# Kernel optimization log

Hardware: AMD Instinct MI355X
Metric: run time of the kernel (lower is better)

The kernel has to match this reference:

```python
import jax, jax.numpy as jnp
import numpy as np
from jax import lax


def bilinear_resize(x, oh, ow):
    # x: (..., H, W); torch F.interpolate bilinear, align_corners=False
    H, W = x.shape[-2], x.shape[-1]
    def coords(n_in, n_out):
        src = (jnp.arange(n_out, dtype=jnp.float32) + 0.5) * (n_in / n_out) - 0.5
        src = jnp.clip(src, 0.0, n_in - 1.0)
        i0 = jnp.floor(src).astype(jnp.int32)
        i1 = jnp.minimum(i0 + 1, n_in - 1)
        return i0, i1, src - i0.astype(jnp.float32)
    r0, r1, wr = coords(H, oh)
    c0, c1, wc = coords(W, ow)
    xr = x[..., r0, :] * (1.0 - wr)[:, None] + x[..., r1, :] * wr[:, None]
    return xr[..., c0] * (1.0 - wc) + xr[..., c1] * wc


def setup_inputs():
    key = jax.random.key(0)
    ks = jax.random.split(key, 20)
    B, D, C, WIN, NH, A = 256, 1280, 64, 14, 8, 49
    def p(k, *sh):
        return jax.random.normal(k, sh, dtype=jnp.float32) * 0.02
    return {
        "X": jax.random.normal(ks[0], (B, 3, D), dtype=jnp.float32),
        "W_embed": p(ks[1], C * WIN * WIN, D), "b_embed": p(ks[2], C * WIN * WIN),
        "W_qkv": p(ks[3], 3 * C, C),
        "W_proj": p(ks[4], C, C), "b_proj": p(ks[5], C),
        "dwc_w": p(ks[6], C, 1, 3, 3), "dwc_b": p(ks[7], C),
        "an_bias": p(ks[8], NH, A, 7, 7), "na_bias": p(ks[9], NH, A, 7, 7),
        "ah_bias": p(ks[10], 1, NH, A, WIN, 1), "aw_bias": p(ks[11], 1, NH, A, 1, WIN),
        "ha_bias": p(ks[12], 1, NH, WIN, 1, A), "wa_bias": p(ks[13], 1, NH, 1, WIN, A),
        "W_adj": p(ks[14], 256, C * WIN * WIN), "b_adj": p(ks[15], 256),
        "W_t1": p(ks[16], 256, D), "b_t1": p(ks[17], 256),
        "W_t2": p(ks[18], 128, 256), "b_t2": p(ks[19], 128),
    }


def reference(X, W_embed, b_embed, W_qkv, W_proj, b_proj, dwc_w, dwc_b,
              an_bias, na_bias, ah_bias, aw_bias, ha_bias, wa_bias,
              W_adj, b_adj, W_t1, b_t1, W_t2, b_t2):
    B = X.shape[0]
    C, WIN, NH, A = 64, 14, 8, 49
    N = WIN * WIN            # 196 tokens
    HD = C // NH             # head dim 8
    scale = HD ** -0.5
    b3 = 3 * B

    # embed_to_img: (B*3, 1280) -> (B*3, C*N) -> tokens (B*3, N, C)
    Xe = X.reshape(b3, -1) @ W_embed.T + b_embed
    xt = Xe.reshape(b3, N, C)

    # AgentAttention
    qkv = xt @ W_qkv.T                                  # (b3, N, 3C), qkv_bias=False
    q, k, v = jnp.split(qkv, 3, axis=-1)
    # agent tokens: AdaptiveAvgPool2d 14x14 -> 7x7 over q (exact 2x2 mean)
    agent = q.reshape(b3, 7, 2, 7, 2, C).mean(axis=(2, 4)).reshape(b3, A, C)
    q = q.reshape(b3, N, NH, HD).transpose(0, 2, 1, 3)
    k = k.reshape(b3, N, NH, HD).transpose(0, 2, 1, 3)
    v = v.reshape(b3, N, NH, HD).transpose(0, 2, 1, 3)
    agent = agent.reshape(b3, A, NH, HD).transpose(0, 2, 1, 3)

    # stage 1: agents attend to all tokens
    pb = bilinear_resize(an_bias, WIN, WIN).reshape(NH, A, N) \
         + (ah_bias + aw_bias).reshape(NH, A, N)
    agent_attn = jax.nn.softmax(jnp.einsum('bhad,bhnd->bhan', agent * scale, k) + pb, axis=-1)
    agent_v = jnp.einsum('bhan,bhnd->bhad', agent_attn, v)   # (b3, NH, A, HD)

    # stage 2: tokens attend to agents
    ab = bilinear_resize(na_bias, WIN, WIN).reshape(NH, A, N).transpose(0, 2, 1) \
         + (ha_bias + wa_bias).reshape(NH, N, A)
    q_attn = jax.nn.softmax(jnp.einsum('bhnd,bhad->bhna', q * scale, agent) + ab, axis=-1)
    o = jnp.einsum('bhna,bhad->bhnd', q_attn, agent_v)
    o = o.transpose(0, 2, 1, 3).reshape(b3, N, C)

    # depthwise conv enhancement on v
    v_img = v.transpose(0, 2, 1, 3).reshape(b3, WIN, WIN, C).transpose(0, 3, 1, 2)
    dwc = lax.conv_general_dilated(v_img, dwc_w, (1, 1), [(1, 1), (1, 1)],
                                   feature_group_count=C) + dwc_b[None, :, None, None]
    o = o + dwc.transpose(0, 2, 3, 1).reshape(b3, N, C)
    o = o @ W_proj.T + b_proj

    X_adj = (o.reshape(b3, -1) @ W_adj.T + b_adj).reshape(B, 3, -1)

    def mlp(z):
        return jnp.tanh(z @ W_t1.T + b_t1) @ W_t2.T + b_t2
    anchor, pos, neg = mlp(X[:, 0]), mlp(X[:, 1]), mlp(X[:, 2])
    return anchor, pos, neg, X_adj
```

## Files before the change

kernel.cpp:

```cpp
#include <hip/hip_runtime.h>

using u16 = unsigned short;
using u32 = unsigned int;

constexpr int Bn   = 256;
constexpr int Dd   = 1280;
constexpr int Cc   = 64;
constexpr int WINc = 14;
constexpr int NHc  = 8;
constexpr int Ac   = 49;
constexpr int Nc   = WINc * WINc;
constexpr int HDc  = Cc / NHc;
constexpr int B3c  = 3 * Bn;
constexpr int CNc  = Cc * Nc;

typedef __attribute__((ext_vector_type(8))) short v8s;
typedef __attribute__((ext_vector_type(4))) float v4f;
typedef __attribute__((ext_vector_type(2))) float v2f;

__device__ __forceinline__ float bflo(u32 u){ union{u32 x; float f;} c; c.x = u << 16; return c.f; }
__device__ __forceinline__ float bfhi(u32 u){ union{u32 x; float f;} c; c.x = u & 0xffff0000u; return c.f; }
__device__ __forceinline__ float bfs(u16 h){ union{u32 x; float f;} c; c.x = ((u32)h) << 16; return c.f; }
__device__ __forceinline__ u16 f2bb(float f){
  u32 u = __float_as_uint(f);
  u32 r = (u + 0x7fffu + ((u >> 16) & 1u)) >> 16;
  return (u16)r;
}
__device__ __forceinline__ void unpack8(uint4 u, float* dst){
  dst[0]=bflo(u.x); dst[1]=bfhi(u.x); dst[2]=bflo(u.y); dst[3]=bfhi(u.y);
  dst[4]=bflo(u.z); dst[5]=bfhi(u.z); dst[6]=bflo(u.w); dst[7]=bfhi(u.w);
}
__device__ __forceinline__ uint4 pack8(const float* s){
  uint4 r;
  r.x = (u32)f2bb(s[0]) | ((u32)f2bb(s[1]) << 16);
  r.y = (u32)f2bb(s[2]) | ((u32)f2bb(s[3]) << 16);
  r.z = (u32)f2bb(s[4]) | ((u32)f2bb(s[5]) << 16);
  r.w = (u32)f2bb(s[6]) | ((u32)f2bb(s[7]) << 16);
  return r;
}

__device__ __forceinline__ void gl_lds16(const u16* g, u16* l){
  __builtin_amdgcn_global_load_lds(
      (const __attribute__((address_space(1))) unsigned int*)g,
      (__attribute__((address_space(3))) unsigned int*)l,
      16, 0, 0);
}

constexpr int WeN   = 12544 * 1280;
constexpr int XN    = 768 * 1280;
constexpr int WadjN = 256 * CNc;
constexpr int W1N   = 256 * 1280;
constexpr int W2N   = 128 * 256;
constexpr int CONVB = (WeN + XN + WadjN + W1N + W2N) / (256*8);
constexpr int BIASB = (2 * NHc * Ac * Nc + 255) / 256;
__global__ __launch_bounds__(256) void conv_bias_kernel(const float* __restrict__ We,
                                                        const float* __restrict__ X,
                                                        const float* __restrict__ Wadj,
                                                        const float* __restrict__ W1,
                                                        const float* __restrict__ W2,
                                                        u16* __restrict__ WeB,
                                                        u16* __restrict__ XB,
                                                        u16* __restrict__ WadjB,
                                                        u16* __restrict__ W1B,
                                                        u16* __restrict__ W2B,
                                                        const float* __restrict__ an, const float* __restrict__ na,
                                                        const float* __restrict__ ah, const float* __restrict__ aw,
                                                        const float* __restrict__ ha, const float* __restrict__ wa,
                                                        float* __restrict__ pb, float* __restrict__ ab)
{
  if (blockIdx.x >= CONVB) {
    const int total = NHc * Ac * Nc;
    int idx = (blockIdx.x - CONVB) * 256 + threadIdx.x;
    if (idx >= 2 * total) return;
    const bool isab = idx >= total;
    const int r = isab ? idx - total : idx;
    const int h = r / (Ac * Nc);
    const int r2 = r % (Ac * Nc);
    int a, n;
    if (isab) { n = r2 / Ac; a = r2 % Ac; } else { a = r2 / Nc; n = r2 % Nc; }
    const int y = n / WINc, x = n % WINc;
    float sy = fminf(fmaxf(0.5f * y - 0.25f, 0.f), 6.f);
    float sx = fminf(fmaxf(0.5f * x - 0.25f, 0.f), 6.f);
    const int y0 = (int)sy, x0 = (int)sx;
    const float wy = sy - y0, wx = sx - x0;
    const int y1 = (y0 + 1 < 6) ? y0 + 1 : 6;
    const int x1 = (x0 + 1 < 6) ? x0 + 1 : 6;
    const float* src = (isab ? na : an) + (h * Ac + a) * 49;
    const float v00 = src[y0*7 + x0], v01 = src[y0*7 + x1];
    const float v10 = src[y1*7 + x0], v11 = src[y1*7 + x1];
    const float bi = (1.f - wy) * ((1.f - wx) * v00 + wx * v01)
                   + wy * ((1.f - wx) * v10 + wx * v11);
    if (!isab) pb[((size_t)h*Nc + n)*Ac + a] = bi + ah[(h*Ac + a)*WINc + y] + aw[(h*Ac + a)*WINc + x];
    else       ab[((size_t)h*Ac + a)*Nc + n] = bi + ha[(h*WINc + y)*Ac + a] + wa[(h*WINc + x)*Ac + a];
    return;
  }
  const size_t idx = ((size_t)blockIdx.x * 256 + threadIdx.x) * 8;
  const float* src; u16* dst;
  if (idx < (size_t)WeN)                          { src = We + idx;                         dst = WeB + idx; }
  else if (idx < (size_t)WeN + XN)                { src = X + (idx - WeN);                  dst = XB + (idx - WeN); }
  else if (idx < (size_t)WeN + XN + WadjN)        { src = Wadj + (idx - WeN - XN);          dst = WadjB + (idx - WeN - XN); }
  else if (idx < (size_t)WeN + XN + WadjN + W1N)  { src = W1 + (idx - WeN - XN - WadjN);    dst = W1B + (idx - WeN - XN - WadjN); }
  else                                            { src = W2 + (idx - WeN - XN - WadjN - W1N); dst = W2B + (idx - WeN - XN - WadjN - W1N); }
  float v[8];
  *reinterpret_cast<float4*>(&v[0]) = *reinterpret_cast<const float4*>(src);
  *reinterpret_cast<float4*>(&v[4]) = *reinterpret_cast<const float4*>(src + 4);
  *reinterpret_cast<uint4*>(dst) = pack8(v);
}

template<int KK, int NN, bool TANH>
__global__ __launch_bounds__(256) void gemm_bf16_t(const u16* __restrict__ Amat,
                                                   const u16* __restrict__ Bmat,
                                                   const float* __restrict__ bias,
                                                   u16* __restrict__ Cmat)
{
  __shared__ u16 As[128 * 32];
  __shared__ u16 Bs[128 * 32];
  const int t = threadIdx.x;
  const int n0 = blockIdx.x * 128, m0 = blockIdx.y * 128;
  const int wave = t >> 6, lane = t & 63;
  const int wm = wave >> 1, wn = wave & 1;
  const int mi = lane & 15, quad = lane >> 4;

  v4f acc[4][4];
  #pragma unroll
  for (int a = 0; a < 4; ++a)
    #pragma unroll
    for (int b = 0; b < 4; ++b) acc[a][b] = (v4f){0.f, 0.f, 0.f, 0.f};

  const int rs = wave*32 + (lane >> 2);
  const int cs = (lane & 3) * 8;
  const u16* ga0 = Amat + (size_t)(m0 + rs) * KK + cs;
  const u16* ga1 = Amat + (size_t)(m0 + rs + 16) * KK + cs;
  const u16* gb0 = Bmat + (size_t)(n0 + rs) * KK + cs;
  const u16* gb1 = Bmat + (size_t)(n0 + rs + 16) * KK + cs;
  u16* la0 = &As[(wave*32)      * 32];
  u16* la1 = &As[(wave*32 + 16) * 32];
  u16* lb0 = &Bs[(wave*32)      * 32];
  u16* lb1 = &Bs[(wave*32 + 16) * 32];

  for (int kt = 0; kt < KK; kt += 32) {
    gl_lds16(ga0 + kt, la0);
    gl_lds16(ga1 + kt, la1);
    gl_lds16(gb0 + kt, lb0);
    gl_lds16(gb1 + kt, lb1);
    __syncthreads();

    v8s af[4], bf[4];
    #pragma unroll
    for (int mt = 0; mt < 4; ++mt)
      af[mt] = *reinterpret_cast<const v8s*>(&As[(wm*64 + mt*16 + mi)*32 + quad*8]);
    #pragma unroll
    for (int nt = 0; nt < 4; ++nt)
      bf[nt] = *reinterpret_cast<const v8s*>(&Bs[(wn*64 + nt*16 + mi)*32 + quad*8]);
    #pragma unroll
    for (int mt = 0; mt < 4; ++mt)
      #pragma unroll
      for (int nt = 0; nt < 4; ++nt)
        acc[mt][nt] = __builtin_amdgcn_mfma_f32_16x16x32_bf16(af[mt], bf[nt], acc[mt][nt], 0, 0, 0);
    __syncthreads();
  }

  #pragma unroll
  for (int nt = 0; nt < 4; ++nt) {
    const int col = n0 + wn*64 + nt*16 + mi;
    const float bc = bias[col];
    #pragma unroll
    for (int mt = 0; mt < 4; ++mt) {
      #pragma unroll
      for (int r = 0; r < 4; ++r) {
        const int row = m0 + wm*64 + mt*16 + quad*4 + r;
        float val = acc[mt][nt][r] + bc;
        if constexpr (TANH) val = tanhf(val);
        Cmat[(size_t)row * NN + col] = f2bb(val);
      }
    }
  }
}

__global__ __launch_bounds__(256) void mlp2_mfma(const u16* __restrict__ H,
                                                 const u16* __restrict__ W2B,
                                                 const float* __restrict__ b2,
                                                 float* __restrict__ outp)
{
  __shared__ u16 As[128 * 40];
  __shared__ u16 Bs[128 * 40];
  const int t = threadIdx.x;
  const int m0 = blockIdx.x * 128;
  const int wave = t >> 6, lane = t & 63;
  const int wm = wave >> 1, wn = wave & 1;
  const int mi = lane & 15, quad = lane >> 4;
  const int srow = t >> 1, scol = (t & 1) * 16;

  v4f acc[4][4];
  #pragma unroll
  for (int a = 0; a < 4; ++a)
    #pragma unroll
    for (int b = 0; b < 4; ++b) acc[a][b] = (v4f){0.f, 0.f, 0.f, 0.f};

  for (int kt = 0; kt < 256; kt += 32) {
    const u16* ap = H + (size_t)(m0 + srow) * 256 + kt + scol;
    *reinterpret_cast<uint4*>(&As[srow*40 + scol])     = *reinterpret_cast<const uint4*>(ap);
    *reinterpret_cast<uint4*>(&As[srow*40 + scol + 8]) = *reinterpret_cast<const uint4*>(ap + 8);
    const u16* bp = W2B + (size_t)srow * 256 + kt + scol;
    *reinterpret_cast<uint4*>(&Bs[srow*40 + scol])     = *reinterpret_cast<const uint4*>(bp);
    *reinterpret_cast<uint4*>(&Bs[srow*40 + scol + 8]) = *reinterpret_cast<const uint4*>(bp + 8);
    __syncthreads();

    v8s af[4], bf[4];
    #pragma unroll
    for (int mt = 0; mt < 4; ++mt)
      af[mt] = *reinterpret_cast<const v8s*>(&As[(wm*64 + mt*16 + mi)*40 + quad*8]);
    #pragma unroll
    for (int nt = 0; nt < 4; ++nt)
      bf[nt] = *reinterpret_cast<const v8s*>(&Bs[(wn*64 + nt*16 + mi)*40 + quad*8]);
    #pragma unroll
    for (int mt = 0; mt < 4; ++mt)
      #pragma unroll
      for (int nt = 0; nt < 4; ++nt)
        acc[mt][nt] = __builtin_amdgcn_mfma_f32_16x16x32_bf16(af[mt], bf[nt], acc[mt][nt], 0, 0, 0);
    __syncthreads();
  }

  #pragma unroll
  for (int nt = 0; nt < 4; ++nt) {
    const int col = wn*64 + nt*16 + mi;
    const float bc = b2[col];
    #pragma unroll
    for (int mt = 0; mt < 4; ++mt) {
      #pragma unroll
      for (int r = 0; r < 4; ++r) {
        const int row = m0 + wm*64 + mt*16 + quad*4 + r;
        const int bi = row / 3, s = row - bi * 3;
        outp[(size_t)s * (Bn*128) + (size_t)bi * 128 + col] = acc[mt][nt][r] + bc;
      }
    }
  }
}

__global__ __launch_bounds__(256) void qkv_mfma(const u16* __restrict__ xt, const float* __restrict__ Wqkv,
                                                u16* __restrict__ qh, u16* __restrict__ kh, u16* __restrict__ vb)
{
  __shared__ u16 As[256 * 72];
  __shared__ u16 Bs[64 * 72];
  const int t = threadIdx.x;
  const int m0 = blockIdx.x * 256;
  const int seg = blockIdx.y;
  const int wave = t >> 6, lane = t & 63;
  const int mi = lane & 15, quad = lane >> 4;

  for (int i = t; i < Cc*Cc; i += 256) {
    const int j = i >> 6, c = i & 63;
    Bs[j*72 + c] = f2bb(Wqkv[(size_t)(seg*64 + j)*64 + c]);
  }
  {
    const int ar = t >> 2, ac = (t & 3) * 16;
    #pragma unroll
    for (int rb = 0; rb < 4; ++rb) {
      const int row = rb*64 + ar;
      const uint4* src = reinterpret_cast<const uint4*>(xt + ((size_t)(m0 + row))*64 + ac);
      *reinterpret_cast<uint4*>(&As[row*72 + ac])     = src[0];
      *reinterpret_cast<uint4*>(&As[row*72 + ac + 8]) = src[1];
    }
  }
  __syncthreads();

  v4f acc[4][4];
  #pragma unroll
  for (int a = 0; a < 4; ++a)
    #pragma unroll
    for (int b = 0; b < 4; ++b) acc[a][b] = (v4f){0.f, 0.f, 0.f, 0.f};

  #pragma unroll
  for (int ks = 0; ks < 2; ++ks) {
    v8s af[4], bf[4];
    #pragma unroll
    for (int mt = 0; mt < 4; ++mt)
      af[mt] = *reinterpret_cast<const v8s*>(&As[(wave*64 + mt*16 + mi)*72 + ks*32 + quad*8]);
    #pragma unroll
    for (int nt = 0; nt < 4; ++nt)
      bf[nt] = *reinterpret_cast<const v8s*>(&Bs[(nt*16 + mi)*72 + ks*32 + quad*8]);
    #pragma unroll
    for (int mt = 0; mt < 4; ++mt)
      #pragma unroll
      for (int nt = 0; nt < 4; ++nt)
        acc[mt][nt] = __builtin_amdgcn_mfma_f32_16x16x32_bf16(af[mt], bf[nt], acc[mt][nt], 0, 0, 0);
  }

  u16* hm = (seg == 0) ? qh : kh;
  #pragma unroll
  for (int nt = 0; nt < 4; ++nt) {
    const int col = nt*16 + mi;
    const int h = col >> 3, d = col & 7;
    #pragma unroll
    for (int mt = 0; mt < 4; ++mt) {
      #pragma unroll
      for (int r = 0; r < 4; ++r) {
        const int row = m0 + wave*64 + mt*16 + quad*4 + r;
        const u16 val = f2bb(acc[mt][nt][r]);
        if (seg < 2) {
          const int b = row / Nc, n = row - b * Nc;
          hm[((size_t)(b*NHc + h)*Nc + n)*8 + d] = val;
        } else {
          vb[(size_t)row * 64 + col] = val;
        }
      }
    }
  }
}

__global__ __launch_bounds__(256) void attn_kernel(const u16* __restrict__ qh, const u16* __restrict__ kh,
                                                   const u16* __restrict__ v,
                                                   const float* __restrict__ pb, const float* __restrict__ ab,
                                                   u16* __restrict__ o)
{
  __shared__ float sU[Nc*10];
  __shared__ float sK[Nc*8], sV[Nc*8];
  __shared__ float sAg[Ac*8], sAV[Ac*8];
  const int bh = blockIdx.x;
  const int b = bh >> 3, h = bh & 7;
  const int t = threadIdx.x;
  const float scale = 0.3535533905932738f;

  float qreg[8];
  if (t < Nc) {
    const size_t base = ((size_t)bh * Nc + t) * 8;
    unpack8(*reinterpret_cast<const uint4*>(qh + base), qreg);
    #pragma unroll
    for (int d = 0; d < 8; ++d) sU[t*8 + d] = qreg[d];
    unpack8(*reinterpret_cast<const uint4*>(kh + base), &sK[t*8]);
    unpack8(*reinterpret_cast<const uint4*>(v + ((size_t)b*Nc + t)*64 + h*8), &sV[t*8]);
  }
  __syncthreads();

  for (int i = t; i < Ac*8; i += 256) {
    const int a = i >> 3, d = i & 7;
    const int ay = a / 7, ax = a % 7;
    const int n00 = (ay * 2) * WINc + ax * 2;
    sAg[i] = 0.25f * (sU[n00*8+d] + sU[(n00+1)*8+d] + sU[(n00+WINc)*8+d] + sU[(n00+WINc+1)*8+d]);
  }
  __syncthreads();

  if (t < Nc) {
    const int qd = t / Ac, a = t - qd * Ac;
    const int nb = qd * Ac;
    v2f g2[4];
    #pragma unroll
    for (int d2 = 0; d2 < 4; ++d2) g2[d2] = *reinterpret_cast<const v2f*>(&sAg[a*8 + d2*2]);
    const float* pbr = pb + ((size_t)h*Nc + nb)*Ac + a;
    float l0 = 0.f, l1 = 0.f;
    v2f avA[4] = {}, avB[4] = {};
    for (int j = 0; j < 48; j += 2) {
      const v2f* k0 = reinterpret_cast<const v2f*>(&sK[(nb + j)*8]);
      const v2f* k1 = reinterpret_cast<const v2f*>(&sK[(nb + j + 1)*8]);
      v2f sa = (g2[0]*k0[0] + g2[1]*k0[1]) + (g2[2]*k0[2] + g2[3]*k0[3]);
      v2f sb = (g2[0]*k1[0] + g2[1]*k1[1]) + (g2[2]*k1[2] + g2[3]*k1[3]);
      const float e0 = __expf((sa.x + sa.y) * scale + pbr[j*Ac]);
      const float e1 = __expf((sb.x + sb.y) * scale + pbr[(j+1)*Ac]);
      l0 += e0; l1 += e1;
      const v2f* v0 = reinterpret_cast<const v2f*>(&sV[(nb + j)*8]);
      const v2f* v1 = reinterpret_cast<const v2f*>(&sV[(nb + j + 1)*8]);
      const v2f e02 = {e0, e0}, e12 = {e1, e1};
      #pragma unroll
      for (int d2 = 0; d2 < 4; ++d2) { avA[d2] += e02 * v0[d2]; avB[d2] += e12 * v1[d2]; }
    }
    {
      const v2f* k0 = reinterpret_cast<const v2f*>(&sK[(nb + 48)*8]);
      v2f sa = (g2[0]*k0[0] + g2[1]*k0[1]) + (g2[2]*k0[2] + g2[3]*k0[3]);
      const float e0 = __expf((sa.x + sa.y) * scale + pbr[48*Ac]);
      l0 += e0;
      const v2f* v0 = reinterpret_cast<const v2f*>(&sV[(nb + 48)*8]);
      const v2f e02 = {e0, e0};
      #pragma unroll
      for (int d2 = 0; d2 < 4; ++d2) avA[d2] += e02 * v0[d2];
    }
    float* pp = &sU[t*9];
    pp[0] = l0 + l1;
    #pragma unroll
    for (int d2 = 0; d2 < 4; ++d2) {
      const v2f m = avA[d2] + avB[d2];
      pp[1+d2*2] = m.x; pp[2+d2*2] = m.y;
    }
  }
  __syncthreads();

  if (t < Ac) {
    float L = 0.f, av[8] = {};
    #pragma unroll
    for (int p = 0; p < 4; ++p) {
      const float* pp = &sU[(p*Ac + t)*9];
      L += pp[0];
      #pragma unroll
      for (int d = 0; d < 8; ++d) av[d] += pp[1+d];
    }
    const float inv = 1.f / L;
    #pragma unroll
    for (int d = 0; d < 8; ++d) sAV[t*8 + d] = av[d] * inv;
  }
  __syncthreads();

  if (t < Nc) {
    v2f q2[4];
    #pragma unroll
    for (int d2 = 0; d2 < 4; ++d2) q2[d2] = (v2f){qreg[d2*2], qreg[d2*2+1]};
    const float* abr = ab + (size_t)h*Ac*Nc + t;
    float l0 = 0.f, l1 = 0.f;
    v2f oA[4] = {}, oB[4] = {};
    for (int a = 0; a < 48; a += 2) {
      const v2f* g0 = reinterpret_cast<const v2f*>(&sAg[a*8]);
      const v2f* g1 = reinterpret_cast<const v2f*>(&sAg[(a+1)*8]);
      v2f sa = (q2[0]*g0[0] + q2[1]*g0[1]) + (q2[2]*g0[2] + q2[3]*g0[3]);
      v2f sb = (q2[0]*g1[0] + q2[1]*g1[1]) + (q2[2]*g1[2] + q2[3]*g1[3]);
      const float e0 = __expf((sa.x + sa.y) * scale + abr[a*Nc]);
      const float e1 = __expf((sb.x + sb.y) * scale + abr[(a+1)*Nc]);
      l0 += e0; l1 += e1;
      const v2f* a0 = reinterpret_cast<const v2f*>(&sAV[a*8]);
      const v2f* a1 = reinterpret_cast<const v2f*>(&sAV[(a+1)*8]);
      const v2f e02 = {e0, e0}, e12 = {e1, e1};
      #pragma unroll
      for (int d2 = 0; d2 < 4; ++d2) { oA[d2] += e02 * a0[d2]; oB[d2] += e12 * a1[d2]; }
    }
    {
      const v2f* g0 = reinterpret_cast<const v2f*>(&sAg[48*8]);
      v2f sa = (q2[0]*g0[0] + q2[1]*g0[1]) + (q2[2]*g0[2] + q2[3]*g0[3]);
      const float e0 = __expf((sa.x + sa.y) * scale + abr[48*Nc]);
      l0 += e0;
      const v2f* a0 = reinterpret_cast<const v2f*>(&sAV[48*8]);
      const v2f e02 = {e0, e0};
      #pragma unroll
      for (int d2 = 0; d2 < 4; ++d2) oA[d2] += e02 * a0[d2];
    }
    const float inv = 1.f / (l0 + l1);
    float o8[8];
    #pragma unroll
    for (int d2 = 0; d2 < 4; ++d2) {
      const v2f m = oA[d2] + oB[d2];
      o8[d2*2] = m.x * inv; o8[d2*2+1] = m.y * inv;
    }
    *reinterpret_cast<uint4*>(&o[((size_t)b*Nc + t)*64 + h*8]) = pack8(o8);
  }
}

__global__ __launch_bounds__(256) void dwc_kernel(const u16* __restrict__ o, const u16* __restrict__ v,
                                                  const float* __restrict__ dwc_w, const float* __restrict__ dwc_b,
                                                  u16* __restrict__ U)
{
  __shared__ u16 sV[Nc*Cc];
  __shared__ float sWw[9*64];
  const int b = blockIdx.x, t = threadIdx.x;

  const uint2* vsrc = reinterpret_cast<const uint2*>(v + (size_t)b * CNc);
  uint2* sV2 = reinterpret_cast<uint2*>(sV);
  for (int i = t; i < CNc/4; i += 256) sV2[i] = vsrc[i];
  for (int i = t; i < 9*64; i += 256) {
    const int k = i >> 6, c = i & 63;
    sWw[i] = dwc_w[c*9 + k];
  }
  __syncthreads();

  const int c0 = (t & 7) * 8;
  float wreg[9][8], breg[8];
  #pragma unroll
  for (int k = 0; k < 9; ++k) {
    *reinterpret_cast<float4*>(&wreg[k][0]) = *reinterpret_cast<const float4*>(&sWw[k*64 + c0]);
    *reinterpret_cast<float4*>(&wreg[k][4]) = *reinterpret_cast<const float4*>(&sWw[k*64 + c0 + 4]);
  }
  *reinterpret_cast<float4*>(&breg[0]) = *reinterpret_cast<const float4*>(dwc_b + c0);
  *reinterpret_cast<float4*>(&breg[4]) = *reinterpret_cast<const float4*>(dwc_b + c0 + 4);

  const u16* ob = o + (size_t)b * CNc;
  u16* ub = U + (size_t)b * CNc;
  for (int i = t; i < CNc/8; i += 256) {
    const int n = i >> 3;
    const int y = n / WINc, x = n % WINc;
    float acc[8], vv[8];
    unpack8(*reinterpret_cast<const uint4*>(ob + (size_t)i*8), acc);
    #pragma unroll
    for (int j = 0; j < 8; ++j) acc[j] += breg[j];
    #pragma unroll
    for (int ky = 0; ky < 3; ++ky) {
      const int yy = y + ky - 1;
      if (yy < 0 || yy >= WINc) continue;
      #pragma unroll
      for (int kx = 0; kx < 3; ++kx) {
        const int xx = x + kx - 1;
        if (xx < 0 || xx >= WINc) continue;
        const int k = ky*3 + kx;
        unpack8(*reinterpret_cast<const uint4*>(&sV[(yy*WINc + xx)*Cc + c0]), vv);
        #pragma unroll
        for (int j = 0; j < 8; ++j) acc[j] = fmaf(wreg[k][j], vv[j], acc[j]);
      }
    }
    *reinterpret_cast<uint4*>(ub + (size_t)i*8) = pack8(acc);
  }
}

__global__ __launch_bounds__(256) void proj_mfma(const u16* __restrict__ U,
                                                 const float* __restrict__ Wp,
                                                 const float* __restrict__ bp,
                                                 u16* __restrict__ oproj)
{
  __shared__ u16 As[256 * 72];
  __shared__ u16 Bs[64 * 72];
  const int t = threadIdx.x;
  const int m0 = blockIdx.x * 256;
  const int wave = t >> 6, lane = t & 63;
  const int mi = lane & 15, quad = lane >> 4;

  for (int i = t; i < Cc*Cc; i += 256) {
    const int j = i >> 6, c = i & 63;
    Bs[j*72 + c] = f2bb(Wp[i]);
  }
  {
    const int ar = t >> 2, ac = (t & 3) * 16;
    #pragma unroll
    for (int rb = 0; rb < 4; ++rb) {
      const int row = rb*64 + ar;
      const uint4* src = reinterpret_cast<const uint4*>(U + ((size_t)(m0 + row))*64 + ac);
      *reinterpret_cast<uint4*>(&As[row*72 + ac])     = src[0];
      *reinterpret_cast<uint4*>(&As[row*72 + ac + 8]) = src[1];
    }
  }
  __syncthreads();

  v4f acc[4][4];
  #pragma unroll
  for (int a = 0; a < 4; ++a)
    #pragma unroll
    for (int b = 0; b < 4; ++b) acc[a][b] = (v4f){0.f, 0.f, 0.f, 0.f};

  #pragma unroll
  for (int ks = 0; ks < 2; ++ks) {
    v8s af[4], bf[4];
    #pragma unroll
    for (int mt = 0; mt < 4; ++mt)
      af[mt] = *reinterpret_cast<const v8s*>(&As[(wave*64 + mt*16 + mi)*72 + ks*32 + quad*8]);
    #pragma unroll
    for (int nt = 0; nt < 4; ++nt)
      bf[nt] = *reinterpret_cast<const v8s*>(&Bs[(nt*16 + mi)*72 + ks*32 + quad*8]);
    #pragma unroll
    for (int mt = 0; mt < 4; ++mt)
      #pragma unroll
      for (int nt = 0; nt < 4; ++nt)
        acc[mt][nt] = __builtin_amdgcn_mfma_f32_16x16x32_bf16(af[mt], bf[nt], acc[mt][nt], 0, 0, 0);
  }

  #pragma unroll
  for (int nt = 0; nt < 4; ++nt) {
    const int col = nt*16 + mi;
    const float bc = bp[col];
    #pragma unroll
    for (int mt = 0; mt < 4; ++mt) {
      #pragma unroll
      for (int r = 0; r < 4; ++r) {
        const int row = m0 + wave*64 + mt*16 + quad*4 + r;
        oproj[(size_t)row * 64 + col] = f2bb(acc[mt][nt][r] + bc);
      }
    }
  }
}

__global__ __launch_bounds__(256) void gemm_adj_mfma(const u16* __restrict__ Amat,
                                                     const u16* __restrict__ BmatB,
                                                     float* __restrict__ part)
{
  constexpr int K = CNc, Kc = CNc/8;
  __shared__ u16 As[128 * 32];
  __shared__ u16 Bs[128 * 32];
  const int t = threadIdx.x;
  const int n0 = blockIdx.x * 128, m0 = blockIdx.y * 128;
  const int kbeg = blockIdx.z * Kc;
  const int wave = t >> 6, lane = t & 63;
  const int wm = wave >> 1, wn = wave & 1;
  const int mi = lane & 15, quad = lane >> 4;

  v4f acc[4][4];
  #pragma unroll
  for (int a = 0; a < 4; ++a)
    #pragma unroll
    for (int b = 0; b < 4; ++b) acc[a][b] = (v4f){0.f, 0.f, 0.f, 0.f};

  const int rs = wave*32 + (lane >> 2);
  const int cs = (lane & 3) * 8;
  const u16* ga0 = Amat + (size_t)(m0 + rs) * K + kbeg + cs;
  const u16* ga1 = Amat + (size_t)(m0 + rs + 16) * K + kbeg + cs;
  const u16* gb0 = BmatB + (size_t)(n0 + rs) * K + kbeg + cs;
  const u16* gb1 = BmatB + (size_t)(n0 + rs + 16) * K + kbeg + cs;
  u16* la0 = &As[(wave*32)      * 32];
  u16* la1 = &As[(wave*32 + 16) * 32];
  u16* lb0 = &Bs[(wave*32)      * 32];
  u16* lb1 = &Bs[(wave*32 + 16) * 32];

  for (int kt = 0; kt < Kc; kt += 32) {
    gl_lds16(ga0 + kt, la0);
    gl_lds16(ga1 + kt, la1);
    gl_lds16(gb0 + kt, lb0);
    gl_lds16(gb1 + kt, lb1);
    __syncthreads();

    v8s af[4], bf[4];
    #pragma unroll
    for (int mt = 0; mt < 4; ++mt)
      af[mt] = *reinterpret_cast<const v8s*>(&As[(wm*64 + mt*16 + mi)*32 + quad*8]);
    #pragma unroll
    for (int nt = 0; nt < 4; ++nt)
      bf[nt] = *reinterpret_cast<const v8s*>(&Bs[(wn*64 + nt*16 + mi)*32 + quad*8]);
    #pragma unroll
    for (int mt = 0; mt < 4; ++mt)
      #pragma unroll
      for (int nt = 0; nt < 4; ++nt)
        acc[mt][nt] = __builtin_amdgcn_mfma_f32_16x16x32_bf16(af[mt], bf[nt], acc[mt][nt], 0, 0, 0);
    __syncthreads();
  }

  const size_t zoff = (size_t)blockIdx.z * B3c * 256;
  #pragma unroll
  for (int nt = 0; nt < 4; ++nt) {
    const int col = n0 + wn*64 + nt*16 + mi;
    #pragma unroll
    for (int mt = 0; mt < 4; ++mt) {
      #pragma unroll
      for (int r = 0; r < 4; ++r) {
        const int row = m0 + wm*64 + mt*16 + quad*4 + r;
        part[zoff + (size_t)row * 256 + col] = acc[mt][nt][r];
      }
    }
  }
}

__global__ __launch_bounds__(256) void reduce_bias_kernel(const float* __restrict__ part,
                                                          const float* __restrict__ bias,
                                                          float* __restrict__ outp)
{
  const int idx = blockIdx.x * 256 + threadIdx.x;
  const int n = idx & 255;
  float acc = bias[n];
  #pragma unroll
  for (int s = 0; s < 8; ++s) acc += part[(size_t)s * B3c * 256 + idx];
  outp[idx] = acc;
}

extern "C" void kernel_launch(void* const* d_in, const int* in_sizes, int n_in,
                              void* d_out, int out_size, void* d_ws, size_t ws_size,
                              hipStream_t stream)
{
  auto in = [&](int i){ return reinterpret_cast<const float*>(d_in[i]); };
  const float *X = in(0), *We = in(1), *be = in(2), *Wq = in(3), *Wp = in(4), *bp = in(5),
              *dww = in(6), *dwb = in(7), *anb = in(8), *nab = in(9), *ahb = in(10), *awb = in(11),
              *hab = in(12), *wab = in(13), *Wadj = in(14), *badj = in(15),
              *W1 = in(16), *b1 = in(17), *W2 = in(18), *b2 = in(19);
  float* out = reinterpret_cast<float*>(d_out);
  char* w = reinterpret_cast<char*>(d_ws);

  const size_t TOK = (size_t)B3c * CNc;
  u16* xt = reinterpret_cast<u16*>(w);
  u16* qh = reinterpret_cast<u16*>(w + TOK*2);
  u16* kh = reinterpret_cast<u16*>(w + TOK*4);
  u16* vb = reinterpret_cast<u16*>(w + TOK*6);
  float* pb = reinterpret_cast<float*>(w + TOK*8);
  float* ab = pb + NHc*Ac*Nc;
  u16* WadjB = reinterpret_cast<u16*>(ab + NHc*Ac*Nc);
  u16* XB  = WadjB + WadjN;
  u16* W1B = XB + XN;
  u16* W2B = W1B + W1N;
  u16* H   = W2B + W2N;
  u16* WeB = qh;
  u16* U = qh;
  float* part = reinterpret_cast<float*>(kh);

  conv_bias_kernel<<<dim3(CONVB + BIASB), 256, 0, stream>>>(
      We, X, Wadj, W1, W2, WeB, XB, WadjB, W1B, W2B,
      anb, nab, ahb, awb, hab, wab, pb, ab);
  gemm_bf16_t<Dd, CNc, false><<<dim3(CNc/128, B3c/128), 256, 0, stream>>>(XB, WeB, be, xt);
  qkv_mfma<<<dim3((B3c*Nc)/256, 3), 256, 0, stream>>>(xt, Wq, qh, kh, vb);
  attn_kernel<<<dim3(B3c*NHc), 256, 0, stream>>>(qh, kh, vb, pb, ab, xt );
  dwc_kernel<<<dim3(B3c), 256, 0, stream>>>(xt , vb, dww, dwb, U);
  proj_mfma<<<dim3((B3c*Nc)/256), 256, 0, stream>>>(U, Wp, bp, xt );
  gemm_adj_mfma<<<dim3(256/128, B3c/128, 8), 256, 0, stream>>>(xt , WadjB, part);
  reduce_bias_kernel<<<dim3((B3c*256)/256), 256, 0, stream>>>(part, badj, out + 3*Bn*128);
  gemm_bf16_t<Dd, 256, true><<<dim3(256/128, B3c/128), 256, 0, stream>>>(XB, W1B, b1, H);
  mlp2_mfma<<<dim3(B3c/128), 256, 0, stream>>>(H, W2B, b2, out);
}
```

Before: 424.9 us.

## Fuse embed and MLP1 GEMMs, loop qkv segments in-block, use exp2 softmax

The separate MLP first-layer GEMM is folded into the embed GEMM launch as extra column blocks, which removes one kernel launch and fills the grid. The qkv kernel now loads its A tile once and loops over the three q/k/v weight segments inside each block, instead of launching three y-blocks that each reload the same A tile. Attention biases are pre-scaled by log2(e) so the softmax can use exp2f with an fma. In exchange, qkv has a third as many blocks, each doing serial work with extra barriers.

```diff
diff --git a/kernel.cpp b/kernel.cpp
--- a/kernel.cpp
+++ b/kernel.cpp
@@ -69,6 +69,7 @@
                                                         float* __restrict__ pb, float* __restrict__ ab)
 {
   if (blockIdx.x >= CONVB) {
+    constexpr float LOG2E = 1.4426950408889634f;
     const int total = NHc * Ac * Nc;
     int idx = (blockIdx.x - CONVB) * 256 + threadIdx.x;
     if (idx >= 2 * total) return;
@@ -90,8 +91,8 @@
     const float v10 = src[y1*7 + x0], v11 = src[y1*7 + x1];
     const float bi = (1.f - wy) * ((1.f - wx) * v00 + wx * v01)
                    + wy * ((1.f - wx) * v10 + wx * v11);
-    if (!isab) pb[((size_t)h*Nc + n)*Ac + a] = bi + ah[(h*Ac + a)*WINc + y] + aw[(h*Ac + a)*WINc + x];
-    else       ab[((size_t)h*Ac + a)*Nc + n] = bi + ha[(h*WINc + y)*Ac + a] + wa[(h*WINc + x)*Ac + a];
+    if (!isab) pb[((size_t)h*Nc + n)*Ac + a] = (bi + ah[(h*Ac + a)*WINc + y] + aw[(h*Ac + a)*WINc + x]) * LOG2E;
+    else       ab[((size_t)h*Ac + a)*Nc + n] = (bi + ha[(h*WINc + y)*Ac + a] + wa[(h*WINc + x)*Ac + a]) * LOG2E;
     return;
   }
   const size_t idx = ((size_t)blockIdx.x * 256 + threadIdx.x) * 8;
@@ -107,16 +108,25 @@
   *reinterpret_cast<uint4*>(dst) = pack8(v);
 }
 
-template<int KK, int NN, bool TANH>
-__global__ __launch_bounds__(256) void gemm_bf16_t(const u16* __restrict__ Amat,
-                                                   const u16* __restrict__ Bmat,
-                                                   const float* __restrict__ bias,
-                                                   u16* __restrict__ Cmat)
-{
+__global__ __launch_bounds__(256) void gemm_embed_mlp1(const u16* __restrict__ XB,
+                                                       const u16* __restrict__ WeB,
+                                                       const u16* __restrict__ W1B,
+                                                       const float* __restrict__ be,
+                                                       const float* __restrict__ b1,
+                                                       u16* __restrict__ xt,
+                                                       u16* __restrict__ H)
+{
+  constexpr int KK = Dd;
   __shared__ u16 As[128 * 32];
   __shared__ u16 Bs[128 * 32];
   const int t = threadIdx.x;
-  const int n0 = blockIdx.x * 128, m0 = blockIdx.y * 128;
+  const bool mlp = blockIdx.x >= 98;
+  const int n0 = (mlp ? (blockIdx.x - 98) : blockIdx.x) * 128;
+  const int m0 = blockIdx.y * 128;
+  const u16* Bmat = mlp ? W1B : WeB;
+  const float* bias = mlp ? b1 : be;
+  u16* Cmat = mlp ? H : xt;
+  const int NN = mlp ? 256 : CNc;
   const int wave = t >> 6, lane = t & 63;
   const int wm = wave >> 1, wn = wave & 1;
   const int mi = lane & 15, quad = lane >> 4;
@@ -129,8 +139,8 @@
 
   const int rs = wave*32 + (lane >> 2);
   const int cs = (lane & 3) * 8;
-  const u16* ga0 = Amat + (size_t)(m0 + rs) * KK + cs;
-  const u16* ga1 = Amat + (size_t)(m0 + rs + 16) * KK + cs;
+  const u16* ga0 = XB + (size_t)(m0 + rs) * KK + cs;
+  const u16* ga1 = XB + (size_t)(m0 + rs + 16) * KK + cs;
   const u16* gb0 = Bmat + (size_t)(n0 + rs) * KK + cs;
   const u16* gb1 = Bmat + (size_t)(n0 + rs + 16) * KK + cs;
   u16* la0 = &As[(wave*32)      * 32];
@@ -170,7 +180,7 @@
       for (int r = 0; r < 4; ++r) {
         const int row = m0 + wm*64 + mt*16 + quad*4 + r;
         float val = acc[mt][nt][r] + bc;
-        if constexpr (TANH) val = tanhf(val);
+        if (mlp) val = tanhf(val);
         Cmat[(size_t)row * NN + col] = f2bb(val);
       }
     }
@@ -244,14 +254,9 @@
   __shared__ u16 Bs[64 * 72];
   const int t = threadIdx.x;
   const int m0 = blockIdx.x * 256;
-  const int seg = blockIdx.y;
   const int wave = t >> 6, lane = t & 63;
   const int mi = lane & 15, quad = lane >> 4;
 
-  for (int i = t; i < Cc*Cc; i += 256) {
-    const int j = i >> 6, c = i & 63;
-    Bs[j*72 + c] = f2bb(Wqkv[(size_t)(seg*64 + j)*64 + c]);
-  }
   {
     const int ar = t >> 2, ac = (t & 3) * 16;
     #pragma unroll
@@ -264,44 +269,58 @@
   }
   __syncthreads();
 
-  v4f acc[4][4];
-  #pragma unroll
-  for (int a = 0; a < 4; ++a)
-    #pragma unroll
-    for (int b = 0; b < 4; ++b) acc[a][b] = (v4f){0.f, 0.f, 0.f, 0.f};
-
-  #pragma unroll
-  for (int ks = 0; ks < 2; ++ks) {
-    v8s af[4], bf[4];
-    #pragma unroll
-    for (int mt = 0; mt < 4; ++mt)
-      af[mt] = *reinterpret_cast<const v8s*>(&As[(wave*64 + mt*16 + mi)*72 + ks*32 + quad*8]);
-    #pragma unroll
-    for (int nt = 0; nt < 4; ++nt)
-      bf[nt] = *reinterpret_cast<const v8s*>(&Bs[(nt*16 + mi)*72 + ks*32 + quad*8]);
-    #pragma unroll
-    for (int mt = 0; mt < 4; ++mt)
+  v8s af[2][4];
+  #pragma unroll
+  for (int ks = 0; ks < 2; ++ks)
+    #pragma unroll
+    for (int mt = 0; mt < 4; ++mt)
+      af[ks][mt] = *reinterpret_cast<const v8s*>(&As[(wave*64 + mt*16 + mi)*72 + ks*32 + quad*8]);
+
+  #pragma unroll 1
+  for (int seg = 0; seg < 3; ++seg) {
+    if (seg) __syncthreads();
+    for (int i = t; i < Cc*Cc; i += 256) {
+      const int j = i >> 6, c = i & 63;
+      Bs[j*72 + c] = f2bb(Wqkv[(size_t)(seg*64 + j)*64 + c]);
+    }
+    __syncthreads();
+
+    v4f acc[4][4];
+    #pragma unroll
+    for (int a = 0; a < 4; ++a)
+      #pragma unroll
+      for (int b = 0; b < 4; ++b) acc[a][b] = (v4f){0.f, 0.f, 0.f, 0.f};
+
+    #pragma unroll
+    for (int ks = 0; ks < 2; ++ks) {
+      v8s bf[4];
       #pragma unroll
       for (int nt = 0; nt < 4; ++nt)
-        acc[mt][nt] = __builtin_amdgcn_mfma_f32_16x16x32_bf16(af[mt], bf[nt], acc[mt][nt], 0, 0, 0);
-  }
-
-  u16* hm = (seg == 0) ? qh : kh;
-  #pragma unroll
-  for (int nt = 0; nt < 4; ++nt) {
-    const int col = nt*16 + mi;
-    const int h = col >> 3, d = col & 7;
-    #pragma unroll
-    for (int mt = 0; mt < 4; ++mt) {
-      #pragma unroll
-      for (int r = 0; r < 4; ++r) {
-        const int row = m0 + wave*64 + mt*16 + quad*4 + r;
-        const u16 val = f2bb(acc[mt][nt][r]);
-        if (seg < 2) {
-          const int b = row / Nc, n = row - b * Nc;
-          hm[((size_t)(b*NHc + h)*Nc + n)*8 + d] = val;
-        } else {
-          vb[(size_t)row * 64 + col] = val;
+        bf[nt] = *reinterpret_cast<const v8s*>(&Bs[(nt*16 + mi)*72 + ks*32 + quad*8]);
+      #pragma unroll
+      for (int mt = 0; mt < 4; ++mt)
+        #pragma unroll
+        for (int nt = 0; nt < 4; ++nt)
+          acc[mt][nt] = __builtin_amdgcn_mfma_f32_16x16x32_bf16(af[ks][mt], bf[nt], acc[mt][nt], 0, 0, 0);
+    }
+
+    u16* hm = (seg == 0) ? qh : kh;
+    #pragma unroll
+    for (int nt = 0; nt < 4; ++nt) {
+      const int col = nt*16 + mi;
+      const int h = col >> 3, d = col & 7;
+      #pragma unroll
+      for (int mt = 0; mt < 4; ++mt) {
+        #pragma unroll
+        for (int r = 0; r < 4; ++r) {
+          const int row = m0 + wave*64 + mt*16 + quad*4 + r;
+          const u16 val = f2bb(acc[mt][nt][r]);
+          if (seg < 2) {
+            const int b = row / Nc, n = row - b * Nc;
+            hm[((size_t)(b*NHc + h)*Nc + n)*8 + d] = val;
+          } else {
+            vb[(size_t)row * 64 + col] = val;
+          }
         }
       }
     }
@@ -319,7 +338,7 @@
   const int bh = blockIdx.x;
   const int b = bh >> 3, h = bh & 7;
   const int t = threadIdx.x;
-  const float scale = 0.3535533905932738f;
+  const float scale2 = 0.3535533905932738f * 1.4426950408889634f;
 
   float qreg[8];
   if (t < Nc) {
@@ -354,8 +373,8 @@
       const v2f* k1 = reinterpret_cast<const v2f*>(&sK[(nb + j + 1)*8]);
       v2f sa = (g2[0]*k0[0] + g2[1]*k0[1]) + (g2[2]*k0[2] + g2[3]*k0[3]);
       v2f sb = (g2[0]*k1[0] + g2[1]*k1[1]) + (g2[2]*k1[2] + g2[3]*k1[3]);
-      const float e0 = __expf((sa.x + sa.y) * scale + pbr[j*Ac]);
-      const float e1 = __expf((sb.x + sb.y) * scale + pbr[(j+1)*Ac]);
+      const float e0 = exp2f(fmaf(sa.x + sa.y, scale2, pbr[j*Ac]));
+      const float e1 = exp2f(fmaf(sb.x + sb.y, scale2, pbr[(j+1)*Ac]));
       l0 += e0; l1 += e1;
       const v2f* v0 = reinterpret_cast<const v2f*>(&sV[(nb + j)*8]);
       const v2f* v1 = reinterpret_cast<const v2f*>(&sV[(nb + j + 1)*8]);
@@ -366,7 +385,7 @@
     {
       const v2f* k0 = reinterpret_cast<const v2f*>(&sK[(nb + 48)*8]);
       v2f sa = (g2[0]*k0[0] + g2[1]*k0[1]) + (g2[2]*k0[2] + g2[3]*k0[3]);
-      const float e0 = __expf((sa.x + sa.y) * scale + pbr[48*Ac]);
+      const float e0 = exp2f(fmaf(sa.x + sa.y, scale2, pbr[48*Ac]));
       l0 += e0;
       const v2f* v0 = reinterpret_cast<const v2f*>(&sV[(nb + 48)*8]);
       const v2f e02 = {e0, e0};
@@ -410,8 +429,8 @@
       const v2f* g1 = reinterpret_cast<const v2f*>(&sAg[(a+1)*8]);
       v2f sa = (q2[0]*g0[0] + q2[1]*g0[1]) + (q2[2]*g0[2] + q2[3]*g0[3]);
       v2f sb = (q2[0]*g1[0] + q2[1]*g1[1]) + (q2[2]*g1[2] + q2[3]*g1[3]);
-      const float e0 = __expf((sa.x + sa.y) * scale + abr[a*Nc]);
-      const float e1 = __expf((sb.x + sb.y) * scale + abr[(a+1)*Nc]);
+      const float e0 = exp2f(fmaf(sa.x + sa.y, scale2, abr[a*Nc]));
+      const float e1 = exp2f(fmaf(sb.x + sb.y, scale2, abr[(a+1)*Nc]));
       l0 += e0; l1 += e1;
       const v2f* a0 = reinterpret_cast<const v2f*>(&sAV[a*8]);
       const v2f* a1 = reinterpret_cast<const v2f*>(&sAV[(a+1)*8]);
@@ -422,7 +441,7 @@
     {
       const v2f* g0 = reinterpret_cast<const v2f*>(&sAg[48*8]);
       v2f sa = (q2[0]*g0[0] + q2[1]*g0[1]) + (q2[2]*g0[2] + q2[3]*g0[3]);
-      const float e0 = __expf((sa.x + sa.y) * scale + abr[48*Nc]);
+      const float e0 = exp2f(fmaf(sa.x + sa.y, scale2, abr[48*Nc]));
       l0 += e0;
       const v2f* a0 = reinterpret_cast<const v2f*>(&sAV[48*8]);
       const v2f e02 = {e0, e0};
@@ -670,13 +689,12 @@
   conv_bias_kernel<<<dim3(CONVB + BIASB), 256, 0, stream>>>(
       We, X, Wadj, W1, W2, WeB, XB, WadjB, W1B, W2B,
       anb, nab, ahb, awb, hab, wab, pb, ab);
-  gemm_bf16_t<Dd, CNc, false><<<dim3(CNc/128, B3c/128), 256, 0, stream>>>(XB, WeB, be, xt);
-  qkv_mfma<<<dim3((B3c*Nc)/256, 3), 256, 0, stream>>>(xt, Wq, qh, kh, vb);
+  gemm_embed_mlp1<<<dim3(100, B3c/128), 256, 0, stream>>>(XB, WeB, W1B, be, b1, xt, H);
+  qkv_mfma<<<dim3((B3c*Nc)/256), 256, 0, stream>>>(xt, Wq, qh, kh, vb);
   attn_kernel<<<dim3(B3c*NHc), 256, 0, stream>>>(qh, kh, vb, pb, ab, xt );
   dwc_kernel<<<dim3(B3c), 256, 0, stream>>>(xt , vb, dww, dwb, U);
   proj_mfma<<<dim3((B3c*Nc)/256), 256, 0, stream>>>(U, Wp, bp, xt );
   gemm_adj_mfma<<<dim3(256/128, B3c/128, 8), 256, 0, stream>>>(xt , WadjB, part);
   reduce_bias_kernel<<<dim3((B3c*256)/256), 256, 0, stream>>>(part, badj, out + 3*Bn*128);
-  gemm_bf16_t<Dd, 256, true><<<dim3(256/128, B3c/128), 256, 0, stream>>>(XB, W1B, b1, H);
   mlp2_mfma<<<dim3(B3c/128), 256, 0, stream>>>(H, W2B, b2, out);
 }
```

Result: no change. 430.7 us (+1.4%).
